# Kernel tuning notes

Measured on AMD Instinct MI355X. Metric: run time of the kernel, lower is better.

Reference implementation:

```python
import jax, jax.numpy as jnp
import numpy as np

HEADS = 6
EPS = 1e-5


def _na_idx(L, k, d):
    # NATTEN-style dilated neighborhood: work within dilation cosets,
    # clamp window to stay inside the image (window shifts at borders).
    i = np.arange(L)
    g = i % d
    p = i // d
    Lg = (L - g + d - 1) // d  # coset length per position
    start = np.clip(p - k // 2, 0, Lg - k)
    j = np.arange(k)
    nbr = g[:, None] + d * (start[:, None] + j[None, :])          # [L,k] neighbor coords
    rel = (start[:, None] + j[None, :]) - p[:, None] + (k - 1)    # [L,k] rpb index in [0,2k-2]
    return jnp.asarray(nbr, jnp.int32), jnp.asarray(rel, jnp.int32)


def _na2d(x, qkv_w, qkv_b, proj_w, proj_b, rpb, heads, k, d):
    # x: [B,H,W,C] NHWC neighborhood attention with relative positional bias
    B, H, W, C = x.shape
    dh = C // heads
    scale = dh ** -0.5
    qkv = (x @ qkv_w + qkv_b).reshape(B, H, W, 3, heads, dh)
    qkv = jnp.transpose(qkv, (3, 0, 4, 1, 2, 5))  # [3,B,h,H,W,dh]
    q, kk, v = qkv[0] * scale, qkv[1], qkv[2]
    nh, rh = _na_idx(H, k, d)
    nw, rw = _na_idx(W, k, d)

    def gather(t):  # [B,h,H,W,dh] -> [B,h,H,W,k,k,dh]
        t = t[:, :, nh]              # [B,h,H,k,W,dh]
        t = t[:, :, :, :, nw]        # [B,h,H,k,W,k,dh]
        return jnp.transpose(t, (0, 1, 2, 4, 3, 5, 6))

    kn, vn = gather(kk), gather(v)
    attn = jnp.einsum('bhxyd,bhxyijd->bhxyij', q, kn)  # [B,h,H,W,k,k]
    bias = rpb[:, rh]                  # [h,H,k,2k-1]
    bias = bias[:, :, :, rw]           # [h,H,k,W,k]
    bias = jnp.transpose(bias, (0, 1, 3, 2, 4))  # [h,H,W,k,k]
    attn = attn + bias[None]
    attn = jax.nn.softmax(attn.reshape(B, heads, H, W, k * k), axis=-1)
    attn = attn.reshape(B, heads, H, W, k, k)
    out = jnp.einsum('bhxyij,bhxyijd->bhxyd', attn, vn)
    out = jnp.transpose(out, (0, 2, 3, 1, 4)).reshape(B, H, W, C)
    return out @ proj_w + proj_b


def _rln(x, w, b, m1_w, m1_b, m2_w, m2_b):
    # Revised LayerNorm: normalize over (C,H,W) per sample; meta1/meta2 are 1x1 convs on std/mean
    mean = jnp.mean(x, axis=(1, 2, 3), keepdims=True)
    std = jnp.sqrt(jnp.mean((x - mean) ** 2, axis=(1, 2, 3), keepdims=True) + EPS)
    out = (x - mean) / std * w + b
    rescale = m1_w[None, :, None, None] * std + m1_b[None, :, None, None]
    rebias = m2_w[None, :, None, None] * mean + m2_b[None, :, None, None]
    return out, rescale, rebias


def _c11(x, w, b):  # 1x1 conv on NCHW == per-pixel linear
    return jnp.einsum('bchw,oc->bohw', x, w) + b[None, :, None, None]


def _gelu(x):
    return jax.nn.gelu(x, approximate=False)


def reference(x, ln_w, ln_b, m1_w, m1_b, m2_w, m2_b, qkv1_w, qkv1_b, proj1_w, proj1_b, rpb1, qkv2_w, qkv2_b, proj2_w, proj2_b, rpb2, mlp_w1, mlp_b1, mlp_w2, mlp_b2, bn_g, bn_b, bn_m, bn_v, pa_w1, pa_b1, pa_w2, pa_b2, ca_w1, ca_b1, ca_w2, ca_b2, m2a_w1, m2a_b1, m2a_w2, m2a_b2):
    # ---- NA block 1 (kernel 7, dilation 1) ----
    sc = x
    y, rs, rb = _rln(x, ln_w, ln_b, m1_w, m1_b, m2_w, m2_b)
    a = _na2d(jnp.transpose(y, (0, 2, 3, 1)), qkv1_w, qkv1_b, proj1_w, proj1_b, rpb1, HEADS, 7, 1)
    x = sc + jnp.transpose(a, (0, 3, 1, 2)) * rs + rb
    # ---- NA block 2 (kernel 5, dilation 8) ----
    sc = x
    y, rs, rb = _rln(x, ln_w, ln_b, m1_w, m1_b, m2_w, m2_b)
    a = _na2d(jnp.transpose(y, (0, 2, 3, 1)), qkv2_w, qkv2_b, proj2_w, proj2_b, rpb2, HEADS, 5, 8)
    x = sc + jnp.transpose(a, (0, 3, 1, 2)) * rs + rb
    # ---- MLP (source reuses the pre-attn2 shortcut `sc`) ----
    y, rs, rb = _rln(x, ln_w, ln_b, m1_w, m1_b, m2_w, m2_b)
    m = _c11(jax.nn.relu(_c11(y, mlp_w1, mlp_b1)), mlp_w2, mlp_b2)
    x = sc + m * rs + rb
    # ---- BN + pixel attention + channel attention + mlp2 ----
    sc = x
    inv = jax.lax.rsqrt(bn_v + EPS)
    y = (x - bn_m[None, :, None, None]) * (inv * bn_g)[None, :, None, None] + bn_b[None, :, None, None]
    pa = jax.nn.sigmoid(_c11(_gelu(_c11(y, pa_w1, pa_b1)), pa_w2, pa_b2))  # [B,1,H,W]
    y = pa * y
    gap = jnp.mean(y, axis=(2, 3), keepdims=True)
    ca = jax.nn.sigmoid(_c11(_gelu(_c11(gap, ca_w1, ca_b1)), ca_w2, ca_b2))  # [B,C,1,1]
    y = ca * y
    y = _c11(_gelu(_c11(y, m2a_w1, m2a_b1)), m2a_w2, m2a_b2)
    return sc + y


def setup_inputs() -> dict:
    key = jax.random.key(0)
    B, C, H, W, HID = 4, 96, 64, 64, 384
    ks = iter(jax.random.split(key, 48))

    def rn(shape, s=0.02):
        return jax.random.normal(next(ks), shape, jnp.float32) * s

    d = {}
    d['x'] = jax.random.normal(next(ks), (B, C, H, W), jnp.float32)
    d['ln_w'] = jnp.ones((1, C, 1, 1), jnp.float32)
    d['ln_b'] = jnp.zeros((1, C, 1, 1), jnp.float32)
    d['m1_w'] = rn((C,)); d['m1_b'] = jnp.ones((C,), jnp.float32)
    d['m2_w'] = rn((C,)); d['m2_b'] = jnp.zeros((C,), jnp.float32)
    d['qkv1_w'] = rn((C, 3 * C)); d['qkv1_b'] = jnp.zeros((3 * C,), jnp.float32)
    d['proj1_w'] = rn((C, C)); d['proj1_b'] = jnp.zeros((C,), jnp.float32)
    d['rpb1'] = rn((HEADS, 13, 13))
    d['qkv2_w'] = rn((C, 3 * C)); d['qkv2_b'] = jnp.zeros((3 * C,), jnp.float32)
    d['proj2_w'] = rn((C, C)); d['proj2_b'] = jnp.zeros((C,), jnp.float32)
    d['rpb2'] = rn((HEADS, 9, 9))
    d['mlp_w1'] = rn((HID, C)); d['mlp_b1'] = jnp.zeros((HID,), jnp.float32)
    d['mlp_w2'] = rn((C, HID)); d['mlp_b2'] = jnp.zeros((C,), jnp.float32)
    d['bn_g'] = jnp.ones((C,), jnp.float32); d['bn_b'] = jnp.zeros((C,), jnp.float32)
    d['bn_m'] = jnp.zeros((C,), jnp.float32); d['bn_v'] = jnp.ones((C,), jnp.float32)
    d['pa_w1'] = rn((C // 8, C)); d['pa_b1'] = jnp.zeros((C // 8,), jnp.float32)
    d['pa_w2'] = rn((1, C // 8)); d['pa_b2'] = jnp.zeros((1,), jnp.float32)
    d['ca_w1'] = rn((C, C)); d['ca_b1'] = jnp.zeros((C,), jnp.float32)
    d['ca_w2'] = rn((C, C)); d['ca_b2'] = jnp.zeros((C,), jnp.float32)
    d['m2a_w1'] = rn((C, C)); d['m2a_b1'] = jnp.zeros((C,), jnp.float32)
    d['m2a_w2'] = rn((C, C)); d['m2a_b2'] = jnp.zeros((C,), jnp.float32)
    return d
```

## Files before the change

### kernel.cpp

```cpp
#include <hip/hip_runtime.h>
#include <math.h>

#define CC 96
#define NP 4096
#define NHEADS 6
#define NELEMF 393216.0f
#define EPSF 1e-5f

typedef __attribute__((ext_vector_type(8))) short bf16x8;
typedef __attribute__((ext_vector_type(4))) float f32x4;
#define MFMA16(a,b,c) __builtin_amdgcn_mfma_f32_16x16x32_bf16(a,b,c,0,0,0)

#define WQKV1  64
#define WQKV2  (WQKV1+13824)
#define WPROJ1 (WQKV2+13824)
#define WPROJ2 (WPROJ1+4608)
#define WMLP1  (WPROJ2+4608)
#define WMLP2  (WMLP1+18432)
#define WM2A1  (WMLP2+18432)
#define WM2A2  (WM2A1+4608)
#define WPA1T  (WM2A2+4608)
#define WBNS   (WPA1T+1152)
#define WCA1T  (WBNS+192)
#define WCA2T  (WCA1T+9216)
#define WS_Q   870784
#define WS_K   (WS_Q+786432)
#define WS_V   (WS_K+786432)
#define WS_ATTPM (WS_V+786432)
#define WS_X1  (WS_ATTPM+786432)
#define WS_X2  (WS_X1+1572864)
#define WS_X3  (WS_X2+1572864)
#define WS_PA  (WS_X3+1572864)
#define WS_GAP (WS_PA+16384)

__device__ __forceinline__ float gelu_f(float x){
  return 0.5f * x * (1.0f + erff(x * 0.7071067811865476f));
}
__device__ __forceinline__ float sigmoid_f(float x){
  return 1.0f / (1.0f + __expf(-x));
}
__device__ __forceinline__ unsigned short bfr(float f){
  unsigned int u = __float_as_uint(f);
  u += 0x7fffu + ((u >> 16) & 1u);
  return (unsigned short)(u >> 16);
}
__device__ __forceinline__ float bflo16(unsigned short u){ return __uint_as_float(((unsigned int)u) << 16); }
__device__ __forceinline__ float bflo(unsigned int u){ return __uint_as_float(u << 16); }
__device__ __forceinline__ float bfhi(unsigned int u){ return __uint_as_float(u & 0xffff0000u); }
__device__ __forceinline__ void get_ms(const float* st, int b, float& mean, float& inv, float& stdv){
  float s = st[b], s2 = st[4+b];
  mean = s * (1.0f/NELEMF);
  float var = fmaxf(s2 * (1.0f/NELEMF) - mean*mean, 0.0f);
  stdv = sqrtf(var + EPSF);
  inv = 1.0f / stdv;
}
__device__ __forceinline__ float ldf(const float* p, int i){ return p[i]; }
__device__ __forceinline__ float ldf(const unsigned short* p, int i){ return bflo16(p[i]); }
__device__ __forceinline__ void load4(const float* p, float4& v){ v = *(const float4*)p; }
__device__ __forceinline__ void load4(const unsigned short* p, float4& v){
  ushort4 u = *(const ushort4*)p;
  v.x = bflo16(u.x); v.y = bflo16(u.y); v.z = bflo16(u.z); v.w = bflo16(u.w);
}

__global__ void prep_stats_kernel(const float* __restrict__ x, float* __restrict__ st,
                             const float* __restrict__ q1, const float* __restrict__ q2,
                             const float* __restrict__ p1, const float* __restrict__ p2,
                             const float* __restrict__ w1, const float* __restrict__ w2,
                             const float* __restrict__ a1, const float* __restrict__ a2,
                             const float* __restrict__ pw1,
                             const float* __restrict__ bg, const float* __restrict__ bb,
                             const float* __restrict__ bm, const float* __restrict__ bv,
                             const float* __restrict__ cw1, const float* __restrict__ cw2,
                             float* __restrict__ ws){
  if(blockIdx.x < 384){
    int b = blockIdx.x / CC, c = blockIdx.x % CC;
    const float4* p4 = (const float4*)(x + (size_t)(b*CC + c)*NP);
    float s = 0.f, s2 = 0.f;
    for(int i = threadIdx.x; i < 1024; i += 256){
      float4 v = p4[i];
      s += v.x + v.y + v.z + v.w;
      s2 = fmaf(v.x, v.x, fmaf(v.y, v.y, fmaf(v.z, v.z, fmaf(v.w, v.w, s2))));
    }
    for(int off = 32; off > 0; off >>= 1){ s += __shfl_down(s, off); s2 += __shfl_down(s2, off); }
    __shared__ float ls[8];
    int wid = threadIdx.x >> 6;
    if((threadIdx.x & 63) == 0){ ls[wid] = s; ls[4+wid] = s2; }
    __syncthreads();
    if(threadIdx.x == 0){
      atomicAdd(&st[b],   ls[0]+ls[1]+ls[2]+ls[3]);
      atomicAdd(&st[4+b], ls[4]+ls[5]+ls[6]+ls[7]);
    }
    return;
  }
  int gid = (blockIdx.x - 384)*256 + threadIdx.x;
  if(gid < 27648){ int n = gid/96, c = gid%96; ((unsigned short*)(ws+WQKV1))[gid] = bfr(q1[c*288+n]); }
  else if(gid < 55296){ int g = gid-27648; int n = g/96, c = g%96; ((unsigned short*)(ws+WQKV2))[g] = bfr(q2[c*288+n]); }
  else if(gid < 64512){ int g = gid-55296; int n = g/96, c = g%96; ((unsigned short*)(ws+WPROJ1))[g] = bfr(p1[c*96+n]); }
  else if(gid < 73728){ int g = gid-64512; int n = g/96, c = g%96; ((unsigned short*)(ws+WPROJ2))[g] = bfr(p2[c*96+n]); }
  else if(gid < 110592){ int g = gid-73728; ((unsigned short*)(ws+WMLP1))[g] = bfr(w1[g]); }
  else if(gid < 147456){ int g = gid-110592; ((unsigned short*)(ws+WMLP2))[g] = bfr(w2[g]); }
  else if(gid < 156672){ int g = gid-147456; ((unsigned short*)(ws+WM2A1))[g] = bfr(a1[g]); }
  else if(gid < 165888){ int g = gid-156672; ((unsigned short*)(ws+WM2A2))[g] = bfr(a2[g]); }
  else if(gid < 167040){ int g = gid-165888; int c = g/12, h = g%12; ws[WPA1T + g] = pw1[h*96+c]; }
  else if(gid < 167136){ int c = gid-167040;
    float sc = rsqrtf(bv[c] + EPSF) * bg[c];
    ws[WBNS + c] = sc;
    ws[WBNS + 96 + c] = bb[c] - bm[c]*sc;
  }
  else if(gid < 167520){ ws[WS_GAP + (gid-167136)] = 0.f; }
  else if(gid < 176736){ int g = gid-167520; int o = g/96, c = g%96; ws[WCA1T + c*96 + o] = cw1[g]; }
  else if(gid < 185952){ int g = gid-176736; int o = g/96, c = g%96; ws[WCA2T + c*96 + o] = cw2[g]; }
}

template<typename AT>
__global__ void __launch_bounds__(512) gemm_qkv_kernel(
    const AT* __restrict__ xin, const float* __restrict__ st,
    const float* __restrict__ lnw, const float* __restrict__ lnb,
    const unsigned short* __restrict__ wT, const float* __restrict__ qb,
    unsigned short* __restrict__ qo, unsigned short* __restrict__ ko, unsigned short* __restrict__ vo){
  __shared__ unsigned short Atl[64*104];
  __shared__ float scl[96], ofs[96];
  int m_base = blockIdx.x*64;
  int b = m_base >> 12, pxl0 = m_base & 4095;
  float mean, inv, stdv; get_ms(st, b, mean, inv, stdv);
  int tid = threadIdx.x;
  if(tid < 96){ float s = inv*lnw[tid]; scl[tid] = s; ofs[tid] = lnb[tid] - mean*s; }
  __syncthreads();
  const AT* src = xin + (size_t)b*CC*NP + pxl0;
  for(int idx = tid; idx < 96*16; idx += 512){
    int c = idx >> 4, p4 = (idx & 15) << 2;
    float4 v; load4(src + (size_t)c*NP + p4, v);
    float s = scl[c], o = ofs[c];
    Atl[(p4+0)*104 + c] = bfr(fmaf(v.x, s, o));
    Atl[(p4+1)*104 + c] = bfr(fmaf(v.y, s, o));
    Atl[(p4+2)*104 + c] = bfr(fmaf(v.z, s, o));
    Atl[(p4+3)*104 + c] = bfr(fmaf(v.w, s, o));
  }
  __syncthreads();
  int w = tid >> 6, lane = tid & 63, ml = lane & 15, q = lane >> 4;
  int row = w & 3, nh = w >> 2;
  const unsigned short* arow = Atl + (row*16 + ml)*104;
  bf16x8 av[3];
  #pragma unroll
  for(int ks = 0; ks < 3; ++ks) av[ks] = *(const bf16x8*)(arow + ks*32 + q*8);
  f32x4 z = {0.f,0.f,0.f,0.f};
  #pragma unroll
  for(int g0 = 0; g0 < 3; ++g0){
    int g = nh*3 + g0;
    f32x4 acc[3] = {z, z, z};
    #pragma unroll
    for(int ks = 0; ks < 3; ++ks){
      #pragma unroll
      for(int gg = 0; gg < 3; ++gg){
        bf16x8 bv = *(const bf16x8*)(wT + (g*48 + gg*16 + ml)*96 + ks*32 + q*8);
        acc[gg] = MFMA16(av[ks], bv, acc[gg]);
      }
    }
    #pragma unroll
    for(int gg = 0; gg < 3; ++gg){
      int nfb = g*48 + gg*16;
      int t = nfb/96, head = (nfb%96) >> 4;
      float scale = (t == 0) ? 0.25f : 1.0f;
      unsigned short* dst = (t == 0) ? qo : (t == 1) ? ko : vo;
      float bias = qb[nfb + ml];
      #pragma unroll
      for(int r = 0; r < 4; ++r){
        int pxl = pxl0 + row*16 + q*4 + r;
        dst[(((size_t)(b*NHEADS + head))*NP + pxl)*16 + ml] = bfr((acc[gg][r] + bias)*scale);
      }
    }
  }
}

template<typename SCT>
__global__ void __launch_bounds__(512) gemm_proj_kernel(
    const unsigned short* __restrict__ attpm, const unsigned short* __restrict__ wT,
    const float* __restrict__ pb, const SCT* __restrict__ scx, const float* __restrict__ st,
    const float* __restrict__ m1w, const float* __restrict__ m1b,
    const float* __restrict__ m2w, const float* __restrict__ m2b,
    unsigned short* __restrict__ dst, float* __restrict__ st_out){
  int w = threadIdx.x >> 6, lane = threadIdx.x & 63;
  int ml = lane & 15, q = lane >> 4;
  int m_base = blockIdx.x*128 + w*16;
  int n0 = blockIdx.y*48;
  f32x4 z = {0.f,0.f,0.f,0.f};
  f32x4 acc[3] = {z, z, z};
  {
    const bf16x8* a0 = (const bf16x8*)(attpm + (size_t)(m_base + ml)*96 + q*8);
    #pragma unroll
    for(int ks = 0; ks < 3; ++ks){
      bf16x8 av0 = a0[ks*4];
      #pragma unroll
      for(int g = 0; g < 3; ++g){
        bf16x8 bv = *(const bf16x8*)(wT + (n0 + g*16 + ml)*96 + ks*32 + q*8);
        acc[g] = MFMA16(av0, bv, acc[g]);
      }
    }
  }
  __shared__ float T[48*133];
  #pragma unroll
  for(int g = 0; g < 3; ++g)
    #pragma unroll
    for(int r = 0; r < 4; ++r)
      T[(g*16 + ml)*133 + w*16 + q*4 + r] = acc[g][r];
  __syncthreads();
  int b = (blockIdx.x*128) >> 12, pxl0 = (blockIdx.x*128) & 4095;
  float mean, inv, stdv; get_ms(st, b, mean, inv, stdv);
  float s = 0.f, s2 = 0.f;
  for(int idx = threadIdx.x; idx < 48*128; idx += 512){
    int row = idx >> 7, px = idx & 127;
    int n = n0 + row;
    float rsf = fmaf(m1w[n], stdv, m1b[n]);
    float rbf = fmaf(m2w[n], mean, m2b[n]);
    int ad = (b*CC + n)*NP + pxl0 + px;
    float val = ldf(scx, ad) + (T[row*133 + px] + pb[n])*rsf + rbf;
    dst[ad] = bfr(val);
    s += val; s2 = fmaf(val, val, s2);
  }
  for(int off = 32; off > 0; off >>= 1){ s += __shfl_down(s, off); s2 += __shfl_down(s2, off); }
  __shared__ float ls[16];
  int wid = threadIdx.x >> 6;
  if((threadIdx.x & 63) == 0){ ls[wid] = s; ls[8+wid] = s2; }
  __syncthreads();
  if(threadIdx.x == 0){
    atomicAdd(&st_out[b],   ls[0]+ls[1]+ls[2]+ls[3]+ls[4]+ls[5]+ls[6]+ls[7]);
    atomicAdd(&st_out[4+b], ls[8]+ls[9]+ls[10]+ls[11]+ls[12]+ls[13]+ls[14]+ls[15]);
  }
}

__global__ void __launch_bounds__(512) gemm_mlp_kernel(
    const unsigned short* __restrict__ xin, const float* __restrict__ st,
    const float* __restrict__ lnw, const float* __restrict__ lnb,
    const unsigned short* __restrict__ w1T, const float* __restrict__ b1,
    const unsigned short* __restrict__ w2T, const float* __restrict__ b2,
    const unsigned short* __restrict__ scx,
    const float* __restrict__ m1w, const float* __restrict__ m1b,
    const float* __restrict__ m2w, const float* __restrict__ m2b,
    float* __restrict__ dst,
    const float* __restrict__ bns, const float* __restrict__ pw1t,
    const float* __restrict__ pb1, const float* __restrict__ pw2,
    const float* __restrict__ pb2, float* __restrict__ pa,
    float* __restrict__ gap){
  __shared__ __align__(16) char smbuf[63488];
  __shared__ float scl[96], ofs[96];
  unsigned short* Atl  = (unsigned short*)smbuf;
  unsigned short* hidL = (unsigned short*)(smbuf + 13312);
  float* T = (float*)(smbuf + 13312);
  float* gpart = (float*)smbuf;
  int m_base = blockIdx.x*64;
  int b = m_base >> 12, pxl0 = m_base & 4095;
  float mean, inv, stdv; get_ms(st, b, mean, inv, stdv);
  int tid = threadIdx.x;
  if(tid < 96){ float s = inv*lnw[tid]; scl[tid] = s; ofs[tid] = lnb[tid] - mean*s; }
  __syncthreads();
  const unsigned short* src = xin + (size_t)b*CC*NP + pxl0;
  for(int idx = tid; idx < 96*16; idx += 512){
    int c = idx >> 4, p4 = (idx & 15) << 2;
    float4 v; load4(src + (size_t)c*NP + p4, v);
    float s = scl[c], o = ofs[c];
    Atl[(p4+0)*104 + c] = bfr(fmaf(v.x, s, o));
    Atl[(p4+1)*104 + c] = bfr(fmaf(v.y, s, o));
    Atl[(p4+2)*104 + c] = bfr(fmaf(v.z, s, o));
    Atl[(p4+3)*104 + c] = bfr(fmaf(v.w, s, o));
  }
  __syncthreads();
  int w = tid >> 6, lane = tid & 63, ml = lane & 15, q = lane >> 4;
  int row = w & 3, nh = w >> 2;
  f32x4 z = {0.f,0.f,0.f,0.f};
  {
    const unsigned short* arow = Atl + (row*16 + ml)*104;
    bf16x8 av[3];
    #pragma unroll
    for(int ks = 0; ks < 3; ++ks) av[ks] = *(const bf16x8*)(arow + ks*32 + q*8);
    #pragma unroll
    for(int g0 = 0; g0 < 4; ++g0){
      int g = nh*4 + g0;
      f32x4 acc[3] = {z, z, z};
      #pragma unroll
      for(int ks = 0; ks < 3; ++ks){
        #pragma unroll
        for(int gg = 0; gg < 3; ++gg){
          bf16x8 bv = *(const bf16x8*)(w1T + (g*48 + gg*16 + ml)*96 + ks*32 + q*8);
          acc[gg] = MFMA16(av[ks], bv, acc[gg]);
        }
      }
      #pragma unroll
      for(int gg = 0; gg < 3; ++gg){
        int n = g*48 + gg*16 + ml;
        float bias = b1[n];
        #pragma unroll
        for(int r = 0; r < 4; ++r)
          hidL[(row*16 + q*4 + r)*392 + n] = bfr(fmaxf(acc[gg][r] + bias, 0.f));
      }
    }
  }
  __syncthreads();
  f32x4 acc2[3] = {z, z, z};
  {
    const unsigned short* arow = hidL + (row*16 + ml)*392;
    #pragma unroll
    for(int ks = 0; ks < 12; ++ks){
      bf16x8 av = *(const bf16x8*)(arow + ks*32 + q*8);
      #pragma unroll
      for(int g0 = 0; g0 < 3; ++g0){
        int g = nh*3 + g0;
        bf16x8 bv = *(const bf16x8*)(w2T + (g*16 + ml)*384 + ks*32 + q*8);
        acc2[g0] = MFMA16(av, bv, acc2[g0]);
      }
    }
  }
  __syncthreads();
  #pragma unroll
  for(int g0 = 0; g0 < 3; ++g0){
    int g = nh*3 + g0;
    #pragma unroll
    for(int r = 0; r < 4; ++r)
      T[(g*16 + ml)*68 + row*16 + q*4 + r] = acc2[g0][r];
  }
  __syncthreads();
  for(int idx = tid; idx < 96*64; idx += 512){
    int n = idx >> 6, px = idx & 63;
    float rsf = fmaf(m1w[n], stdv, m1b[n]);
    float rbf = fmaf(m2w[n], mean, m2b[n]);
    int ad = (b*CC + n)*NP + pxl0 + px;
    float val = ldf(scx, ad) + (T[n*68 + px] + b2[n])*rsf + rbf;
    dst[ad] = val;
    T[n*68 + px] = val;
  }
  __syncthreads();
  int pxq = tid >> 3, t = tid & 7;
  float yvv[12], acc[12];
  #pragma unroll
  for(int h = 0; h < 12; ++h) acc[h] = 0.f;
  #pragma unroll 6
  for(int cc = 0; cc < 12; ++cc){
    int c = t*12 + cc;
    float yv = fmaf(T[c*68 + pxq], bns[c], bns[96 + c]);
    yvv[cc] = yv;
    #pragma unroll
    for(int h = 0; h < 12; ++h) acc[h] = fmaf(yv, pw1t[c*12 + h], acc[h]);
  }
  #pragma unroll
  for(int h = 0; h < 12; ++h){
    acc[h] += __shfl_xor(acc[h], 1);
    acc[h] += __shfl_xor(acc[h], 2);
    acc[h] += __shfl_xor(acc[h], 4);
  }
  float s = pb2[0];
  #pragma unroll
  for(int h = 0; h < 12; ++h) s = fmaf(gelu_f(acc[h] + pb1[h]), pw2[h], s);
  float pav = sigmoid_f(s);
  if(t == 0) pa[b*NP + pxl0 + pxq] = pav;
  #pragma unroll 6
  for(int cc = 0; cc < 12; ++cc){
    float g = yvv[cc] * pav;
    g += __shfl_xor(g, 8);  g += __shfl_xor(g, 16); g += __shfl_xor(g, 32);
    if(lane < 8) gpart[w*96 + lane*12 + cc] = g;
  }
  __syncthreads();
  if(tid < 96){
    int c = tid;
    float v = 0.f;
    #pragma unroll
    for(int ww = 0; ww < 8; ++ww) v += gpart[ww*96 + c];
    atomicAdd(&gap[b*96 + c], v * (1.0f/4096.0f));
  }
}

__global__ void __launch_bounds__(512) gemm_m2a_kernel(
    const float* __restrict__ x3, const float* __restrict__ bns,
    const float* __restrict__ pa, const float* __restrict__ gap,
    const float* __restrict__ cw1T, const float* __restrict__ cb1,
    const float* __restrict__ cw2T, const float* __restrict__ cb2,
    const unsigned short* __restrict__ w1T, const float* __restrict__ b1,
    const unsigned short* __restrict__ w2T, const float* __restrict__ b2,
    const float* __restrict__ scx, float* __restrict__ outp){
  __shared__ __align__(16) char smbuf[26624];
  __shared__ float scl[96], ofs[96], pal[64];
  __shared__ float gl[96], tl[96];
  unsigned short* Atl = (unsigned short*)smbuf;
  unsigned short* tl2 = (unsigned short*)(smbuf + 13312);
  float* T = (float*)smbuf;
  int m_base = blockIdx.x*64;
  int b = m_base >> 12, pxl0 = m_base & 4095;
  int tid = threadIdx.x;
  if(tid < 96) gl[tid] = gap[b*96 + tid];
  if(tid >= 128 && tid < 192) pal[tid-128] = pa[m_base + (tid-128)];
  __syncthreads();
  if(tid < 96){
    float a = cb1[tid];
    #pragma unroll 8
    for(int c = 0; c < 96; ++c) a = fmaf(gl[c], cw1T[c*96 + tid], a);
    tl[tid] = gelu_f(a);
  }
  __syncthreads();
  if(tid < 96){
    float a = cb2[tid];
    #pragma unroll 8
    for(int c = 0; c < 96; ++c) a = fmaf(tl[c], cw2T[c*96 + tid], a);
    float cv = sigmoid_f(a);
    scl[tid] = bns[tid]*cv; ofs[tid] = bns[96+tid]*cv;
  }
  __syncthreads();
  const float* src = x3 + (size_t)b*CC*NP + pxl0;
  for(int idx = tid; idx < 96*16; idx += 512){
    int c = idx >> 4, p4 = (idx & 15) << 2;
    float4 v = *(const float4*)(src + (size_t)c*NP + p4);
    float s = scl[c], o = ofs[c];
    Atl[(p4+0)*104 + c] = bfr(fmaf(v.x, s, o) * pal[p4+0]);
    Atl[(p4+1)*104 + c] = bfr(fmaf(v.y, s, o) * pal[p4+1]);
    Atl[(p4+2)*104 + c] = bfr(fmaf(v.z, s, o) * pal[p4+2]);
    Atl[(p4+3)*104 + c] = bfr(fmaf(v.w, s, o) * pal[p4+3]);
  }
  __syncthreads();
  int w = tid >> 6, lane = tid & 63, ml = lane & 15, q = lane >> 4;
  int row = w & 3, nh = w >> 2;
  f32x4 z = {0.f,0.f,0.f,0.f};
  f32x4 acc1[3] = {z, z, z};
  {
    const unsigned short* arow = Atl + (row*16 + ml)*104;
    #pragma unroll
    for(int ks = 0; ks < 3; ++ks){
      bf16x8 av = *(const bf16x8*)(arow + ks*32 + q*8);
      #pragma unroll
      for(int g0 = 0; g0 < 3; ++g0){
        int g = nh*3 + g0;
        bf16x8 bv = *(const bf16x8*)(w1T + (g*16 + ml)*96 + ks*32 + q*8);
        acc1[g0] = MFMA16(av, bv, acc1[g0]);
      }
    }
  }
  #pragma unroll
  for(int g0 = 0; g0 < 3; ++g0){
    int g = nh*3 + g0;
    float bias = b1[g*16 + ml];
    #pragma unroll
    for(int r = 0; r < 4; ++r)
      tl2[(row*16 + q*4 + r)*104 + g*16 + ml] = bfr(gelu_f(acc1[g0][r] + bias));
  }
  __syncthreads();
  f32x4 acc2[3] = {z, z, z};
  {
    const unsigned short* arow = tl2 + (row*16 + ml)*104;
    #pragma unroll
    for(int ks = 0; ks < 3; ++ks){
      bf16x8 av = *(const bf16x8*)(arow + ks*32 + q*8);
      #pragma unroll
      for(int g0 = 0; g0 < 3; ++g0){
        int g = nh*3 + g0;
        bf16x8 bv = *(const bf16x8*)(w2T + (g*16 + ml)*96 + ks*32 + q*8);
        acc2[g0] = MFMA16(av, bv, acc2[g0]);
      }
    }
  }
  __syncthreads();
  #pragma unroll
  for(int g0 = 0; g0 < 3; ++g0){
    int g = nh*3 + g0;
    #pragma unroll
    for(int r = 0; r < 4; ++r)
      T[(g*16 + ml)*68 + row*16 + q*4 + r] = acc2[g0][r];
  }
  __syncthreads();
  for(int idx = tid; idx < 96*64; idx += 512){
    int n = idx >> 6, p = idx & 63;
    int ad = (b*CC + n)*NP + pxl0 + p;
    outp[ad] = scx[ad] + T[n*68 + p] + b2[n];
  }
}

template<int K, int D, int RPB>
__global__ void __launch_bounds__(256) attn_kernel(
    const unsigned short* __restrict__ qb, const unsigned short* __restrict__ kb,
    const unsigned short* __restrict__ vb, const float* __restrict__ rpb,
    unsigned short* __restrict__ outp){
  int bh = blockIdx.x >> 6;
  int x = blockIdx.x & 63;
  int head = bh % NHEADS, b = bh / NHEADS;

  int gx = x % D, px = x / D;
  int Lgx = (64 - gx + D - 1) / D;
  int sx = min(max(px - K/2, 0), Lgx - K);

  __shared__ unsigned int sm[2*K*512];
  unsigned int* kl = sm;
  unsigned int* vl = sm + K*512;
  const unsigned int* kg = (const unsigned int*)(kb + (size_t)bh*NP*16);
  const unsigned int* vg = (const unsigned int*)(vb + (size_t)bh*NP*16);
  int tid = threadIdx.x;
  #pragma unroll
  for(int i = 0; i < K; ++i){
    int hh = gx + D*(sx + i);
    ((uint2*)(kl + i*512))[tid] = ((const uint2*)(kg + hh*512))[tid];
    ((uint2*)(vl + i*512))[tid] = ((const uint2*)(vg + hh*512))[tid];
  }
  __syncthreads();

  int pixoff = tid >> 2, t = tid & 3;
  int y = pixoff;
  int pix = x*64 + y;
  uint2 qd = *(const uint2*)(qb + ((size_t)bh*NP + pix)*16 + 4*t);
  float qx = bflo(qd.x), qy = bfhi(qd.x), qz = bflo(qd.y), qw = bfhi(qd.y);

  int gy = y % D, py = y / D;
  int Lgy = (64 - gy + D - 1) / D;
  int sy = min(max(py - K/2, 0), Lgy - K);

  float sc[K*K];
  #pragma unroll
  for(int i = 0; i < K; ++i){
    #pragma unroll
    for(int j = 0; j < K; ++j){
      int ww = gy + D*(sy + j);
      uint2 kv = *(const uint2*)(kl + i*512 + ww*8 + t*2);
      float s = qx*bflo(kv.x);
      s = fmaf(qy, bfhi(kv.x), s);
      s = fmaf(qz, bflo(kv.y), s);
      s = fmaf(qw, bfhi(kv.y), s);
      sc[i*K + j] = s;
    }
  }
  float mx = -1e30f;
  #pragma unroll
  for(int i = 0; i < K; ++i){
    const float* brow = rpb + (head*RPB + (sx + i - px + (K-1)))*RPB + (sy - py + (K-1));
    #pragma unroll
    for(int j = 0; j < K; ++j){
      float s = sc[i*K + j];
      s += __shfl_xor(s, 1);
      s += __shfl_xor(s, 2);
      s += brow[j];
      sc[i*K + j] = s;
      mx = fmaxf(mx, s);
    }
  }
  float sum = 0.f;
  #pragma unroll
  for(int n = 0; n < K*K; ++n){ float e = __expf(sc[n] - mx); sc[n] = e; sum += e; }
  float rs = 1.0f / sum;
  float4 acc = {0,0,0,0};
  #pragma unroll
  for(int i = 0; i < K; ++i){
    #pragma unroll
    for(int j = 0; j < K; ++j){
      int ww = gy + D*(sy + j);
      float wgt = sc[i*K + j] * rs;
      uint2 vv = *(const uint2*)(vl + i*512 + ww*8 + t*2);
      acc.x = fmaf(wgt, bflo(vv.x), acc.x);
      acc.y = fmaf(wgt, bfhi(vv.x), acc.y);
      acc.z = fmaf(wgt, bflo(vv.y), acc.z);
      acc.w = fmaf(wgt, bfhi(vv.y), acc.w);
    }
  }
  ushort4 o4;
  o4.x = bfr(acc.x); o4.y = bfr(acc.y); o4.z = bfr(acc.z); o4.w = bfr(acc.w);
  *(ushort4*)(outp + ((size_t)(b*NP + pix))*96 + head*16 + 4*t) = o4;
}

extern "C" void kernel_launch(void* const* d_in, const int* in_sizes, int n_in,
                              void* d_out, int out_size, void* d_ws, size_t ws_size,
                              hipStream_t stream){
  (void)in_sizes; (void)n_in; (void)out_size; (void)ws_size;
  const float* x     = (const float*)d_in[0];
  const float* lnw   = (const float*)d_in[1];
  const float* lnb   = (const float*)d_in[2];
  const float* m1w   = (const float*)d_in[3];
  const float* m1b   = (const float*)d_in[4];
  const float* m2w   = (const float*)d_in[5];
  const float* m2b   = (const float*)d_in[6];
  const float* qkv1w = (const float*)d_in[7];
  const float* qkv1b = (const float*)d_in[8];
  const float* proj1w= (const float*)d_in[9];
  const float* proj1b= (const float*)d_in[10];
  const float* rpb1  = (const float*)d_in[11];
  const float* qkv2w = (const float*)d_in[12];
  const float* qkv2b = (const float*)d_in[13];
  const float* proj2w= (const float*)d_in[14];
  const float* proj2b= (const float*)d_in[15];
  const float* rpb2  = (const float*)d_in[16];
  const float* mw1   = (const float*)d_in[17];
  const float* mb1   = (const float*)d_in[18];
  const float* mw2   = (const float*)d_in[19];
  const float* mb2   = (const float*)d_in[20];
  const float* bng   = (const float*)d_in[21];
  const float* bnb   = (const float*)d_in[22];
  const float* bnm   = (const float*)d_in[23];
  const float* bnv   = (const float*)d_in[24];
  const float* paw1  = (const float*)d_in[25];
  const float* pab1  = (const float*)d_in[26];
  const float* paw2  = (const float*)d_in[27];
  const float* pab2  = (const float*)d_in[28];
  const float* caw1  = (const float*)d_in[29];
  const float* cab1  = (const float*)d_in[30];
  const float* caw2  = (const float*)d_in[31];
  const float* cab2  = (const float*)d_in[32];
  const float* aw1   = (const float*)d_in[33];
  const float* ab1   = (const float*)d_in[34];
  const float* aw2   = (const float*)d_in[35];
  const float* ab2   = (const float*)d_in[36];

  float* ws  = (float*)d_ws;
  float* out = (float*)d_out;
  float* st0 = ws;
  float* st1 = ws + 8;
  float* st2 = ws + 16;
  unsigned short* q     = (unsigned short*)(ws + WS_Q);
  unsigned short* k     = (unsigned short*)(ws + WS_K);
  unsigned short* v     = (unsigned short*)(ws + WS_V);
  unsigned short* attpm = (unsigned short*)(ws + WS_ATTPM);
  unsigned short* x1b   = (unsigned short*)(ws + WS_X1);
  unsigned short* x2b   = (unsigned short*)(ws + WS_X2);
  float* x3  = ws + WS_X3;
  float* pab = ws + WS_PA;
  float* gpb = ws + WS_GAP;
  float* bns = ws + WBNS;

  hipMemsetAsync(d_ws, 0, 64*sizeof(float), stream);
  prep_stats_kernel<<<1111, 256, 0, stream>>>(x, st0, qkv1w, qkv2w, proj1w, proj2w,
                                              mw1, mw2, aw1, aw2, paw1,
                                              bng, bnb, bnm, bnv, caw1, caw2, ws);

  gemm_qkv_kernel<float><<<256, 512, 0, stream>>>(x, st0, lnw, lnb,
      (unsigned short*)(ws+WQKV1), qkv1b, q, k, v);
  attn_kernel<7,1,13><<<1536, 256, 0, stream>>>(q, k, v, rpb1, attpm);
  gemm_proj_kernel<float><<<dim3(128,2), 512, 0, stream>>>(attpm, (unsigned short*)(ws+WPROJ1),
      proj1b, x, st0, m1w, m1b, m2w, m2b, x1b, st1);

  gemm_qkv_kernel<unsigned short><<<256, 512, 0, stream>>>(x1b, st1, lnw, lnb,
      (unsigned short*)(ws+WQKV2), qkv2b, q, k, v);
  attn_kernel<5,8,9><<<1536, 256, 0, stream>>>(q, k, v, rpb2, attpm);
  gemm_proj_kernel<unsigned short><<<dim3(128,2), 512, 0, stream>>>(attpm, (unsigned short*)(ws+WPROJ2),
      proj2b, x1b, st1, m1w, m1b, m2w, m2b, x2b, st2);

  gemm_mlp_kernel<<<256, 512, 0, stream>>>(x2b, st2, lnw, lnb,
      (unsigned short*)(ws+WMLP1), mb1, (unsigned short*)(ws+WMLP2), mb2,
      x1b, m1w, m1b, m2w, m2b, x3,
      bns, ws + WPA1T, pab1, paw2, pab2, pab, gpb);

  gemm_m2a_kernel<<<256, 512, 0, stream>>>(x3, bns, pab, gpb,
                                           ws + WCA1T, cab1, ws + WCA2T, cab2,
                                           (unsigned short*)(ws+WM2A1), ab1,
                                           (unsigned short*)(ws+WM2A2), ab2, x3, out);
}
```

Baseline: 264.5 us.

## Restructure neighborhood attention to one thread per pixel with shared K/V row reuse

Rewrites the attention kernel so each block handles four query rows and stages the union of their neighbor K/V rows (SPAN rows) in LDS once, instead of reloading K rows per single query row. Each thread now owns a full 16-dim head vector, which removes the 4-lane shuffle reductions and the redundant softmax work previously done by every lane. The RPB table is also staged in LDS. The grid shrinks to 384 blocks, which may reduce occupancy and latency hiding. Register pressure rises from the 16-wide accumulators plus the score arrays, and the transposed LDS layout may cause bank conflicts.

Result: no change. 263.6 us (-0.4%).

```diff
diff --git a/kernel.cpp b/kernel.cpp
--- a/kernel.cpp
+++ b/kernel.cpp
@@ -60,6 +60,31 @@
 __device__ __forceinline__ void load4(const unsigned short* p, float4& v){
   ushort4 u = *(const ushort4*)p;
   v.x = bflo16(u.x); v.y = bflo16(u.y); v.z = bflo16(u.z); v.w = bflo16(u.w);
+}
+
+__device__ __forceinline__ float dot16(const float* qv, const uint2* col, int ww){
+  uint2 a0 = col[ww], a1 = col[64+ww], a2 = col[128+ww], a3 = col[192+ww];
+  float s;
+  s  = qv[0]*bflo(a0.x);           s = fmaf(qv[1],  bfhi(a0.x), s);
+  s = fmaf(qv[2],  bflo(a0.y), s); s = fmaf(qv[3],  bfhi(a0.y), s);
+  s = fmaf(qv[4],  bflo(a1.x), s); s = fmaf(qv[5],  bfhi(a1.x), s);
+  s = fmaf(qv[6],  bflo(a1.y), s); s = fmaf(qv[7],  bfhi(a1.y), s);
+  s = fmaf(qv[8],  bflo(a2.x), s); s = fmaf(qv[9],  bfhi(a2.x), s);
+  s = fmaf(qv[10], bflo(a2.y), s); s = fmaf(qv[11], bfhi(a2.y), s);
+  s = fmaf(qv[12], bflo(a3.x), s); s = fmaf(qv[13], bfhi(a3.x), s);
+  s = fmaf(qv[14], bflo(a3.y), s); s = fmaf(qv[15], bfhi(a3.y), s);
+  return s;
+}
+__device__ __forceinline__ void pv16(float w, const uint2* col, int ww, float* acc){
+  uint2 a0 = col[ww], a1 = col[64+ww], a2 = col[128+ww], a3 = col[192+ww];
+  acc[0]  = fmaf(w, bflo(a0.x), acc[0]);  acc[1]  = fmaf(w, bfhi(a0.x), acc[1]);
+  acc[2]  = fmaf(w, bflo(a0.y), acc[2]);  acc[3]  = fmaf(w, bfhi(a0.y), acc[3]);
+  acc[4]  = fmaf(w, bflo(a1.x), acc[4]);  acc[5]  = fmaf(w, bfhi(a1.x), acc[5]);
+  acc[6]  = fmaf(w, bflo(a1.y), acc[6]);  acc[7]  = fmaf(w, bfhi(a1.y), acc[7]);
+  acc[8]  = fmaf(w, bflo(a2.x), acc[8]);  acc[9]  = fmaf(w, bfhi(a2.x), acc[9]);
+  acc[10] = fmaf(w, bflo(a2.y), acc[10]); acc[11] = fmaf(w, bfhi(a2.y), acc[11]);
+  acc[12] = fmaf(w, bflo(a3.x), acc[12]); acc[13] = fmaf(w, bfhi(a3.x), acc[13]);
+  acc[14] = fmaf(w, bflo(a3.y), acc[14]); acc[15] = fmaf(w, bfhi(a3.y), acc[15]);
 }
 
 __global__ void prep_stats_kernel(const float* __restrict__ x, float* __restrict__ st,
@@ -469,92 +494,96 @@
   }
 }
 
-template<int K, int D, int RPB>
-__global__ void __launch_bounds__(256) attn_kernel(
+template<int K, int D, int RPB, int SPAN>
+__global__ void __launch_bounds__(256) attn2_kernel(
     const unsigned short* __restrict__ qb, const unsigned short* __restrict__ kb,
     const unsigned short* __restrict__ vb, const float* __restrict__ rpb,
     unsigned short* __restrict__ outp){
-  int bh = blockIdx.x >> 6;
-  int x = blockIdx.x & 63;
+  __shared__ uint2 kst[SPAN*256];
+  __shared__ uint2 vst[SPAN*256];
+  __shared__ float rpbl[RPB*RPB];
+  int bh = blockIdx.x >> 4;
+  int quad = blockIdx.x & 15;
   int head = bh % NHEADS, b = bh / NHEADS;
-
-  int gx = x % D, px = x / D;
+  int tid = threadIdx.x;
+  int tcol = tid >> 6, y = tid & 63;
+
+  int gx, px, px0;
+  if(D == 1){ gx = 0; px = quad*4 + tcol; px0 = quad*4; }
+  else      { gx = quad & (D-1); px = (quad >> 3)*4 + tcol; px0 = (quad >> 3)*4; }
   int Lgx = (64 - gx + D - 1) / D;
   int sx = min(max(px - K/2, 0), Lgx - K);
-
-  __shared__ unsigned int sm[2*K*512];
-  unsigned int* kl = sm;
-  unsigned int* vl = sm + K*512;
-  const unsigned int* kg = (const unsigned int*)(kb + (size_t)bh*NP*16);
-  const unsigned int* vg = (const unsigned int*)(vb + (size_t)bh*NP*16);
-  int tid = threadIdx.x;
-  #pragma unroll
-  for(int i = 0; i < K; ++i){
-    int hh = gx + D*(sx + i);
-    ((uint2*)(kl + i*512))[tid] = ((const uint2*)(kg + hh*512))[tid];
-    ((uint2*)(vl + i*512))[tid] = ((const uint2*)(vg + hh*512))[tid];
-  }
-  __syncthreads();
-
-  int pixoff = tid >> 2, t = tid & 3;
-  int y = pixoff;
+  int sxmin = min(max(px0 - K/2, 0), Lgx - K);
+  int nstage = min(SPAN, Lgx - sxmin);
+
+  for(int i = tid; i < RPB*RPB; i += 256) rpbl[i] = rpb[head*RPB*RPB + i];
+  {
+    const uint2* kg = (const uint2*)(kb + (size_t)bh*NP*16);
+    const uint2* vg = (const uint2*)(vb + (size_t)bh*NP*16);
+    int spx = tid & 63, sq = tid >> 6;
+    for(int c = 0; c < nstage; ++c){
+      int hh = gx + D*(sxmin + c);
+      kst[c*256 + sq*64 + spx] = kg[hh*256 + spx*4 + sq];
+      vst[c*256 + sq*64 + spx] = vg[hh*256 + spx*4 + sq];
+    }
+  }
+  int x = gx + D*px;
   int pix = x*64 + y;
-  uint2 qd = *(const uint2*)(qb + ((size_t)bh*NP + pix)*16 + 4*t);
-  float qx = bflo(qd.x), qy = bfhi(qd.x), qz = bflo(qd.y), qw = bfhi(qd.y);
-
-  int gy = y % D, py = y / D;
+  float qv[16];
+  {
+    const uint4* qg = (const uint4*)(qb + ((size_t)bh*NP + pix)*16);
+    uint4 qa = qg[0], qb4 = qg[1];
+    qv[0]=bflo(qa.x);  qv[1]=bfhi(qa.x);  qv[2]=bflo(qa.y);  qv[3]=bfhi(qa.y);
+    qv[4]=bflo(qa.z);  qv[5]=bfhi(qa.z);  qv[6]=bflo(qa.w);  qv[7]=bfhi(qa.w);
+    qv[8]=bflo(qb4.x); qv[9]=bfhi(qb4.x); qv[10]=bflo(qb4.y);qv[11]=bfhi(qb4.y);
+    qv[12]=bflo(qb4.z);qv[13]=bfhi(qb4.z);qv[14]=bflo(qb4.w);qv[15]=bfhi(qb4.w);
+  }
+  __syncthreads();
+
+  int gy = y & (D-1), py = (D==1) ? y : (y >> 3);
   int Lgy = (64 - gy + D - 1) / D;
   int sy = min(max(py - K/2, 0), Lgy - K);
+  int dxb = sx - px + (K-1);
+  int dyb = sy - py + (K-1);
+  int ci0 = sx - sxmin;
 
   float sc[K*K];
   #pragma unroll
   for(int i = 0; i < K; ++i){
+    const uint2* kc = kst + (ci0 + i)*256;
+    const float* br = rpbl + (i + dxb)*RPB + dyb;
     #pragma unroll
     for(int j = 0; j < K; ++j){
       int ww = gy + D*(sy + j);
-      uint2 kv = *(const uint2*)(kl + i*512 + ww*8 + t*2);
-      float s = qx*bflo(kv.x);
-      s = fmaf(qy, bfhi(kv.x), s);
-      s = fmaf(qz, bflo(kv.y), s);
-      s = fmaf(qw, bfhi(kv.y), s);
-      sc[i*K + j] = s;
+      sc[i*K + j] = dot16(qv, kc, ww) + br[j];
     }
   }
   float mx = -1e30f;
   #pragma unroll
-  for(int i = 0; i < K; ++i){
-    const float* brow = rpb + (head*RPB + (sx + i - px + (K-1)))*RPB + (sy - py + (K-1));
-    #pragma unroll
-    for(int j = 0; j < K; ++j){
-      float s = sc[i*K + j];
-      s += __shfl_xor(s, 1);
-      s += __shfl_xor(s, 2);
-      s += brow[j];
-      sc[i*K + j] = s;
-      mx = fmaxf(mx, s);
-    }
-  }
+  for(int n = 0; n < K*K; ++n) mx = fmaxf(mx, sc[n]);
   float sum = 0.f;
   #pragma unroll
   for(int n = 0; n < K*K; ++n){ float e = __expf(sc[n] - mx); sc[n] = e; sum += e; }
   float rs = 1.0f / sum;
-  float4 acc = {0,0,0,0};
+  float acc[16];
+  #pragma unroll
+  for(int d = 0; d < 16; ++d) acc[d] = 0.f;
   #pragma unroll
   for(int i = 0; i < K; ++i){
+    const uint2* vc = vst + (ci0 + i)*256;
     #pragma unroll
     for(int j = 0; j < K; ++j){
       int ww = gy + D*(sy + j);
-      float wgt = sc[i*K + j] * rs;
-      uint2 vv = *(const uint2*)(vl + i*512 + ww*8 + t*2);
-      acc.x = fmaf(wgt, bflo(vv.x), acc.x);
-      acc.y = fmaf(wgt, bfhi(vv.x), acc.y);
-      acc.z = fmaf(wgt, bflo(vv.y), acc.z);
-      acc.w = fmaf(wgt, bfhi(vv.y), acc.w);
-    }
-  }
-  ushort4 o4;
-  o4.x = bfr(acc.x); o4.y = bfr(acc.y); o4.z = bfr(acc.z); o4.w = bfr(acc.w);
-  *(ushort4*)(outp + ((size_t)(b*NP + pix))*96 + head*16 + 4*t) = o4;
+      pv16(sc[i*K + j] * rs, vc, ww, acc);
+    }
+  }
+  unsigned int ow[8];
+  #pragma unroll
+  for(int p = 0; p < 8; ++p)
+    ow[p] = (unsigned int)bfr(acc[2*p]) | ((unsigned int)bfr(acc[2*p+1]) << 16);
+  unsigned short* op = outp + ((size_t)(b*NP + pix))*96 + head*16;
+  ((uint4*)op)[0] = make_uint4(ow[0], ow[1], ow[2], ow[3]);
+  ((uint4*)op)[1] = make_uint4(ow[4], ow[5], ow[6], ow[7]);
 }
 
 extern "C" void kernel_launch(void* const* d_in, const int* in_sizes, int n_in,
@@ -622,13 +651,13 @@
 
   gemm_qkv_kernel<float><<<256, 512, 0, stream>>>(x, st0, lnw, lnb,
       (unsigned short*)(ws+WQKV1), qkv1b, q, k, v);
-  attn_kernel<7,1,13><<<1536, 256, 0, stream>>>(q, k, v, rpb1, attpm);
+  attn2_kernel<7,1,13,10><<<384, 256, 0, stream>>>(q, k, v, rpb1, attpm);
   gemm_proj_kernel<float><<<dim3(128,2), 512, 0, stream>>>(attpm, (unsigned short*)(ws+WPROJ1),
       proj1b, x, st0, m1w, m1b, m2w, m2b, x1b, st1);
 
   gemm_qkv_kernel<unsigned short><<<256, 512, 0, stream>>>(x1b, st1, lnw, lnb,
       (unsigned short*)(ws+WQKV2), qkv2b, q, k, v);
-  attn_kernel<5,8,9><<<1536, 256, 0, stream>>>(q, k, v, rpb2, attpm);
+  attn2_kernel<5,8,9,6><<<384, 256, 0, stream>>>(q, k, v, rpb2, attpm);
   gemm_proj_kernel<unsigned short><<<dim3(128,2), 512, 0, stream>>>(attpm, (unsigned short*)(ws+WPROJ2),
       proj2b, x1b, st1, m1w, m1b, m2w, m2b, x2b, st2);
 
```
